# Kernel optimization log

Hardware: AMD Instinct MI355X
Metric: run time of the kernel (lower is better)

## Reference

```python
import jax, jax.numpy as jnp
import numpy as np

N = 100_000
E = 1_600_000
IN, HID, OUT, ED = 128, 128, 64, 16
NEG_SLOPE = 0.2  # PyG GATConv default leaky_relu slope


def segment_softmax(logits, seg, num_segments):
    m = jax.ops.segment_max(logits, seg, num_segments=num_segments)
    m = jnp.where(jnp.isfinite(m), m, 0.0)
    e = jnp.exp(logits - m[seg])
    s = jax.ops.segment_sum(e, seg, num_segments=num_segments)
    return e / (s[seg] + 1e-16)


def gat_conv(x, edge_index, W, a_src, a_dst, b, edge_attr=None, We=None, ae=None):
    """PyG GATConv, heads=1, add_self_loops=True, fill_value='mean'."""
    n = x.shape[0]
    h = x @ W  # [N, C]
    loop = jnp.arange(n, dtype=edge_index.dtype)
    src = jnp.concatenate([edge_index[0], loop])  # [E+N]
    dst = jnp.concatenate([edge_index[1], loop])
    alpha = (h * a_src).sum(-1)[src] + (h * a_dst).sum(-1)[dst]  # [E+N]
    if edge_attr is not None:
        # self-loop edge_attr filled with per-destination mean (PyG fill_value='mean')
        cnt = jax.ops.segment_sum(jnp.ones((edge_attr.shape[0],), edge_attr.dtype), edge_index[1], num_segments=n)
        mean_attr = jax.ops.segment_sum(edge_attr, edge_index[1], num_segments=n) / jnp.maximum(cnt, 1.0)[:, None]
        ea = jnp.concatenate([edge_attr, mean_attr], axis=0)  # [E+N, ED]
        alpha = alpha + (ea @ We) @ ae
    alpha = jax.nn.leaky_relu(alpha, NEG_SLOPE)
    alpha = segment_softmax(alpha, dst, n)
    out = jax.ops.segment_sum(alpha[:, None] * h[src], dst, num_segments=n)  # scatter-add
    return out + b


def setup_inputs() -> dict:
    key = jax.random.key(0)
    ks = iter(jax.random.split(key, 32))
    g = lambda shape, fan: (jax.random.normal(next(ks), shape, jnp.float32) * (1.0 / np.sqrt(fan)))
    inp = {
        "x": jax.random.normal(next(ks), (N, IN), jnp.float32),
        "edge_index": jax.random.randint(next(ks), (2, E), 0, N, jnp.int32),
        "edge_attr": jax.random.normal(next(ks), (E, ED), jnp.float32),
        # conv1 (no edge_attr)
        "W1": g((IN, HID), IN), "a1_src": g((HID,), HID), "a1_dst": g((HID,), HID), "b1": jnp.zeros((HID,), jnp.float32),
        # conv2 (with edge_attr)
        "W2": g((HID, HID), HID), "a2_src": g((HID,), HID), "a2_dst": g((HID,), HID), "b2": jnp.zeros((HID,), jnp.float32),
        "We2": g((ED, HID), ED), "ae2": g((HID,), HID),
        # initial residual linear
        "Wr": g((IN, HID), IN), "br": jnp.zeros((HID,), jnp.float32),
        # conv_mu
        "Wmu": g((HID, OUT), HID), "amu_src": g((OUT,), OUT), "amu_dst": g((OUT,), OUT), "bmu": jnp.zeros((OUT,), jnp.float32),
        "Wemu": g((ED, OUT), ED), "aemu": g((OUT,), OUT),
        # conv_logstd
        "Wls": g((HID, OUT), HID), "als_src": g((OUT,), OUT), "als_dst": g((OUT,), OUT), "bls": jnp.zeros((OUT,), jnp.float32),
        "Wels": g((ED, OUT), ED), "aels": g((OUT,), OUT),
    }
    return inp


def reference(x, edge_index, edge_attr,
              W1, a1_src, a1_dst, b1,
              W2, a2_src, a2_dst, b2, We2, ae2,
              Wr, br,
              Wmu, amu_src, amu_dst, bmu, Wemu, aemu,
              Wls, als_src, als_dst, bls, Wels, aels):
    h = jax.nn.relu(gat_conv(x, edge_index, W1, a1_src, a1_dst, b1))
    h = jax.nn.relu(gat_conv(h, edge_index, W2, a2_src, a2_dst, b2, edge_attr, We2, ae2))
    h = h + (x @ Wr + br)  # initial residual
    mu = gat_conv(h, edge_index, Wmu, amu_src, amu_dst, bmu, edge_attr, Wemu, aemu)
    logstd = gat_conv(h, edge_index, Wls, als_src, als_dst, bls, edge_attr, Wels, aels)
    return mu, logstd
```

## Files before the change

kernel.cpp:

```cpp
#include <hip/hip_runtime.h>

#define NN 100000
#define NE 1600000
#define BSH 9
#define NBUK 196

typedef __attribute__((ext_vector_type(8))) short bf16x8;
typedef __attribute__((ext_vector_type(4))) float f32x4;

__device__ __forceinline__ float wave_sum(float v){
  #pragma unroll
  for (int o = 32; o; o >>= 1) v += __shfl_xor(v, o, 64);
  return v;
}
__device__ __forceinline__ float grp_sum16(float v){
  #pragma unroll
  for (int o = 8; o; o >>= 1) v += __shfl_xor(v, o, 16);
  return v;
}
__device__ __forceinline__ float bf2f(unsigned short x){
  return __uint_as_float(((unsigned)x) << 16);
}
__device__ __forceinline__ unsigned short f2bf(float f){
  unsigned u = __float_as_uint(f);
  return (unsigned short)((u + 0x7FFFu + ((u >> 16) & 1u)) >> 16);
}

__global__ void prep_w_kernel(const float* __restrict__ W1, const float* __restrict__ W2,
                              const float* __restrict__ Wr, const float* __restrict__ Wmu,
                              const float* __restrict__ Wls,
                              unsigned short* __restrict__ W1t, unsigned short* __restrict__ W2t,
                              unsigned short* __restrict__ Wrt, unsigned short* __restrict__ Wmlt){
  int b = blockIdx.x, t = threadIdx.x;
  for (int it = 0; it < 64; it++){
    int idx = it*256 + t;
    int k = idx >> 7, c = idx & 127;
    float v; unsigned short* dst;
    if (b == 0){ v = W1[k*128+c]; dst = W1t; }
    else if (b == 1){ v = W2[k*128+c]; dst = W2t; }
    else if (b == 2){ v = Wr[k*128+c]; dst = Wrt; }
    else { v = (c & 1) ? Wls[k*64 + (c>>1)] : Wmu[k*64 + (c>>1)]; dst = Wmlt; }
    dst[c*128 + k] = f2bf(v);
  }
}

__global__ void wvec_kernel(const float* __restrict__ We2, const float* __restrict__ ae2,
                            const float* __restrict__ Wemu, const float* __restrict__ aemu,
                            const float* __restrict__ Wels, const float* __restrict__ aels,
                            float* __restrict__ wv){
  int t = threadIdx.x;
  if (t < 16){
    float s = 0.f; for (int c = 0; c < 128; c++) s += We2[t*128+c]*ae2[c];
    wv[t] = s;
  } else if (t < 32){
    int k = t-16; float s = 0.f; for (int c = 0; c < 64; c++) s += Wemu[k*64+c]*aemu[c];
    wv[16+k] = s;
  } else if (t < 48){
    int k = t-32; float s = 0.f; for (int c = 0; c < 64; c++) s += Wels[k*64+c]*aels[c];
    wv[32+k] = s;
  }
}

__global__ void cast_x_kernel(const float* __restrict__ x, unsigned short* __restrict__ Xb){
  int i = blockIdx.x*256 + threadIdx.x;
  if (i >= NN*128/8) return;
  const float4* src = (const float4*)x + (size_t)i*2;
  float4 v0 = src[0], v1 = src[1];
  ushort4 o0 = make_ushort4(f2bf(v0.x), f2bf(v0.y), f2bf(v0.z), f2bf(v0.w));
  ushort4 o1 = make_ushort4(f2bf(v1.x), f2bf(v1.y), f2bf(v1.z), f2bf(v1.w));
  *(ushort4*)(Xb + (size_t)i*8)     = o0;
  *(ushort4*)(Xb + (size_t)i*8 + 4) = o1;
}

__global__ void zero_kernel(int* __restrict__ p, int n){
  int i = blockIdx.x*256 + threadIdx.x;
  if (i < n) p[i] = 0;
}

__global__ __launch_bounds__(1024) void ehist_kernel(const int* __restrict__ ei,
                                                     unsigned* __restrict__ gbcnt){
  __shared__ unsigned h[256];
  int t = threadIdx.x;
  if (t < 256) h[t] = 0;
  __syncthreads();
  int e0 = blockIdx.x*4096 + t;
  #pragma unroll
  for (int k = 0; k < 4; k++){
    int e = e0 + k*1024;
    if (e < NE) atomicAdd(&h[ei[NE+e] >> BSH], 1);
  }
  __syncthreads();
  if (t < 256 && h[t]) atomicAdd(&gbcnt[t], h[t]);
}

__global__ void bscan_kernel(const unsigned* __restrict__ gbcnt,
                             unsigned* __restrict__ gbbase, int* __restrict__ rowptr){
  __shared__ unsigned sh[256];
  int t = threadIdx.x;
  unsigned v = gbcnt[t];
  sh[t] = v; __syncthreads();
  for (int o = 1; o < 256; o <<= 1){
    unsigned add = (t >= o) ? sh[t-o] : 0;
    __syncthreads();
    sh[t] += add;
    __syncthreads();
  }
  gbbase[t+1] = sh[t];
  if (t == 0){ gbbase[0] = 0; rowptr[NN] = NE; }
}

__global__ __launch_bounds__(1024) void bin_kernel(const int* __restrict__ ei,
                                                   const float* __restrict__ ea,
                                                   const float* __restrict__ wv,
                                                   const unsigned* __restrict__ gbbase,
                                                   unsigned* __restrict__ gbfill,
                                                   uint2* __restrict__ bdu,
                                                   float4* __restrict__ bw){
  __shared__ unsigned hcnt[256], hbase[256], hcur[256];
  __shared__ float wvs[48];
  int t = threadIdx.x;
  if (t < 256){ hcnt[t] = 0; hcur[t] = 0; }
  else if (t >= 256 && t < 304) wvs[t-256] = wv[t-256];
  __syncthreads();
  int d[4], u[4], b[4]; float4 w[4]; bool val[4];
  int e0 = blockIdx.x*4096 + t;
  #pragma unroll
  for (int k = 0; k < 4; k++){
    int e = e0 + k*1024;
    val[k] = e < NE;
    if (val[k]){
      d[k] = ei[NE+e]; u[k] = ei[e];
      b[k] = d[k] >> BSH;
      atomicAdd(&hcnt[b[k]], 1);
      const float4* p = (const float4*)(ea + (size_t)e*16);
      float a[16]; float4 vv;
      vv = p[0]; a[0]=vv.x; a[1]=vv.y; a[2]=vv.z; a[3]=vv.w;
      vv = p[1]; a[4]=vv.x; a[5]=vv.y; a[6]=vv.z; a[7]=vv.w;
      vv = p[2]; a[8]=vv.x; a[9]=vv.y; a[10]=vv.z; a[11]=vv.w;
      vv = p[3]; a[12]=vv.x; a[13]=vv.y; a[14]=vv.z; a[15]=vv.w;
      float s2 = 0.f, smu = 0.f, sls = 0.f;
      #pragma unroll
      for (int q = 0; q < 16; q++){
        s2  = fmaf(a[q], wvs[q],    s2);
        smu = fmaf(a[q], wvs[16+q], smu);
        sls = fmaf(a[q], wvs[32+q], sls);
      }
      w[k] = make_float4(s2, smu, sls, 0.f);
    }
  }
  __syncthreads();
  if (t < 256){
    unsigned c = hcnt[t];
    hbase[t] = c ? atomicAdd(&gbfill[t], c) : 0u;
  }
  __syncthreads();
  #pragma unroll
  for (int k = 0; k < 4; k++){
    if (val[k]){
      unsigned pos = atomicAdd(&hcur[b[k]], 1);
      unsigned slot = gbbase[b[k]] + hbase[b[k]] + pos;
      bdu[slot] = make_uint2((unsigned)d[k], (unsigned)u[k]);
      bw[slot]  = w[k];
    }
  }
}

__global__ __launch_bounds__(1024) void place_kernel(const uint2* __restrict__ bdu,
                                                     const float4* __restrict__ bw,
                                                     const unsigned* __restrict__ gbbase,
                                                     int* __restrict__ rowptr,
                                                     unsigned* __restrict__ csr_u,
                                                     float* __restrict__ ewp2,
                                                     float2* __restrict__ ewpmuls){
  __shared__ unsigned h[512], incl[512], cur[512];
  int b = blockIdx.x, t = threadIdx.x;
  unsigned cbase = gbbase[b];
  unsigned cnt = gbbase[b+1] - cbase;
  if (t < 512) h[t] = 0;
  __syncthreads();
  for (unsigned i = t; i < cnt; i += 1024)
    atomicAdd(&h[bdu[cbase+i].x & 511], 1);
  __syncthreads();
  if (t < 512) incl[t] = h[t];
  __syncthreads();
  for (int o = 1; o < 512; o <<= 1){
    unsigned add = (t >= o && t < 512) ? incl[t-o] : 0;
    __syncthreads();
    if (t < 512) incl[t] += add;
    __syncthreads();
  }
  if (t < 512){
    cur[t] = 0;
    int node = (b << BSH) + t;
    if (node < NN) rowptr[node] = (int)(cbase + incl[t] - h[t]);
  }
  __syncthreads();
  for (unsigned i = t; i < cnt; i += 1024){
    uint2 du = bdu[cbase+i];
    unsigned ld = du.x & 511;
    unsigned pos = atomicAdd(&cur[ld], 1);
    unsigned slot = cbase + (incl[ld] - h[ld]) + pos;
    float4 w = bw[cbase+i];
    csr_u[slot] = du.y;
    ewp2[slot] = w.x;
    ewpmuls[slot] = make_float2(w.y, w.z);
  }
}

template<bool OUTF32>
__global__ __launch_bounds__(256) void gemm_bf16(const unsigned short* __restrict__ Xb,
                                                 const unsigned short* __restrict__ Wt,
                                                 void* __restrict__ Y,
                                                 const float* __restrict__ bias, int nrows){
  __shared__ uint4 As[128*16];
  __shared__ uint4 Bs[128*16];
  int t = threadIdx.x;
  int row0 = blockIdx.x * 128;
  #pragma unroll
  for (int p = 0; p < 8; p++){
    int idx = p*256 + t;
    int r = idx >> 4, cir = idx & 15;
    uint4 v = make_uint4(0,0,0,0);
    if (row0 + r < nrows) v = *(const uint4*)(Xb + ((size_t)(row0+r))*128 + cir*8);
    As[r*16 + (cir ^ (r & 7))] = v;
  }
  #pragma unroll
  for (int p = 0; p < 8; p++){
    int idx = p*256 + t;
    int r = idx >> 4, cir = idx & 15;
    Bs[r*16 + (cir ^ (r & 7))] = *(const uint4*)(Wt + (size_t)r*128 + cir*8);
  }
  __syncthreads();
  int w = t >> 6, l = t & 63;
  int lr = l & 15;
  int lk = l >> 4;
  const bf16x8* As8 = (const bf16x8*)As;
  const bf16x8* Bs8 = (const bf16x8*)Bs;
  f32x4 acc[2][8];
  f32x4 zero = {0.f, 0.f, 0.f, 0.f};
  #pragma unroll
  for (int m = 0; m < 2; m++)
    #pragma unroll
    for (int n = 0; n < 8; n++) acc[m][n] = zero;
  #pragma unroll
  for (int ks = 0; ks < 4; ks++){
    bf16x8 a0, a1, bf[8];
    { int r = w*32 + lr;      a0 = As8[r*16 + ((ks*4+lk) ^ (r&7))]; }
    { int r = w*32 + 16 + lr; a1 = As8[r*16 + ((ks*4+lk) ^ (r&7))]; }
    #pragma unroll
    for (int nt = 0; nt < 8; nt++){
      int r = nt*16 + lr;
      bf[nt] = Bs8[r*16 + ((ks*4+lk) ^ (r&7))];
    }
    #pragma unroll
    for (int nt = 0; nt < 8; nt++){
      acc[0][nt] = __builtin_amdgcn_mfma_f32_16x16x32_bf16(a0, bf[nt], acc[0][nt], 0, 0, 0);
      acc[1][nt] = __builtin_amdgcn_mfma_f32_16x16x32_bf16(a1, bf[nt], acc[1][nt], 0, 0, 0);
    }
  }
  #pragma unroll
  for (int mt = 0; mt < 2; mt++){
    int gr0 = row0 + w*32 + mt*16 + lk*4;
    #pragma unroll
    for (int nt = 0; nt < 8; nt++){
      int col = nt*16 + lr;
      float bv = OUTF32 ? bias[col] : 0.f;
      #pragma unroll
      for (int i = 0; i < 4; i++){
        int r = gr0 + i;
        if (r < nrows){
          float o = acc[mt][nt][i];
          if constexpr (OUTF32) ((float*)Y)[(size_t)r*128 + col] = o + bv;
          else ((unsigned short*)Y)[(size_t)r*128 + col] = f2bf(o);
        }
      }
    }
  }
}

__global__ __launch_bounds__(256) void dots_kernel(const unsigned short* __restrict__ Hb,
                                                   const float* __restrict__ asrc,
                                                   const float* __restrict__ adst,
                                                   float* __restrict__ s, float* __restrict__ d){
  int n = (blockIdx.x * blockDim.x + threadIdx.x) >> 6;
  int lane = threadIdx.x & 63;
  if (n >= NN) return;
  ushort2 q = *(const ushort2*)(Hb + (size_t)n*128 + lane*2);
  float h0 = bf2f(q.x), h1 = bf2f(q.y);
  float ps = h0*asrc[lane*2] + h1*asrc[lane*2+1];
  float pd = h0*adst[lane*2] + h1*adst[lane*2+1];
  ps = wave_sum(ps); pd = wave_sum(pd);
  if (lane == 0){ s[n] = ps; d[n] = pd; }
}

__global__ __launch_bounds__(256) void dots_muls_kernel(const unsigned short* __restrict__ Yb,
                                                        const float* __restrict__ amus,
                                                        const float* __restrict__ amud,
                                                        const float* __restrict__ alss,
                                                        const float* __restrict__ alsd,
                                                        float2* __restrict__ sg,
                                                        float2* __restrict__ dg){
  int n = (blockIdx.x * blockDim.x + threadIdx.x) >> 6;
  int lane = threadIdx.x & 63;
  if (n >= NN) return;
  ushort2 q = *(const ushort2*)(Yb + (size_t)n*128 + lane*2);
  float hmu = bf2f(q.x), hls = bf2f(q.y);
  float smu = wave_sum(hmu * amus[lane]);
  float dmu = wave_sum(hmu * amud[lane]);
  float sls = wave_sum(hls * alss[lane]);
  float dls = wave_sum(hls * alsd[lane]);
  if (lane == 0){ sg[n] = make_float2(smu, sls); dg[n] = make_float2(dmu, dls); }
}

template<bool HAS_EW>
__global__ __launch_bounds__(256) void agg_conv(const unsigned short* __restrict__ Hb,
                                                const float* __restrict__ s,
                                                const float* __restrict__ dsc,
                                                const float* __restrict__ ewp,
                                                const int* __restrict__ rowptr,
                                                const unsigned* __restrict__ csr_u,
                                                const float* __restrict__ bias,
                                                const float* __restrict__ resid,
                                                unsigned short* __restrict__ out){
  int v = (blockIdx.x * blockDim.x + threadIdx.x) >> 4;
  int lig = threadIdx.x & 15;
  if (v >= NN) return;
  int rs = rowptr[v], re = rowptr[v+1];
  int deg = re - rs;
  float d_v = dsc[v];
  float acc[8] = {0.f,0.f,0.f,0.f,0.f,0.f,0.f,0.f};
  float pl = 0.f, ewl = 0.f;
  for (int base = rs; base < re; base += 16){
    int i = base + lig;
    int u = 0; float w = 0.f;
    if (i < re){
      u = (int)csr_u[i];
      float e = HAS_EW ? ewp[i] : 0.f;
      if (HAS_EW) ewl += e;
      float a = s[u] + d_v + e;
      float l = a > 0.f ? a : 0.2f*a;
      w = __expf(l);
    }
    pl += w;
    int nv = re - base; if (nv > 16) nv = 16;
    int j = 0;
    for (; j + 4 <= nv; j += 4){
      uint4 q[4]; float wj[4];
      #pragma unroll
      for (int k = 0; k < 4; k++){
        int uk = __shfl(u, j+k, 16);
        wj[k] = __shfl(w, j+k, 16);
        q[k] = *(const uint4*)(Hb + (size_t)uk*128 + lig*8);
      }
      #pragma unroll
      for (int k = 0; k < 4; k++){
        const unsigned* qq = (const unsigned*)&q[k];
        #pragma unroll
        for (int c = 0; c < 4; c++){
          acc[2*c]   = fmaf(wj[k], __uint_as_float(qq[c] << 16), acc[2*c]);
          acc[2*c+1] = fmaf(wj[k], __uint_as_float(qq[c] & 0xFFFF0000u), acc[2*c+1]);
        }
      }
    }
    for (; j < nv; j++){
      int uk = __shfl(u, j, 16);
      float wk = __shfl(w, j, 16);
      uint4 q = *(const uint4*)(Hb + (size_t)uk*128 + lig*8);
      const unsigned* qq = (const unsigned*)&q;
      #pragma unroll
      for (int c = 0; c < 4; c++){
        acc[2*c]   = fmaf(wk, __uint_as_float(qq[c] << 16), acc[2*c]);
        acc[2*c+1] = fmaf(wk, __uint_as_float(qq[c] & 0xFFFF0000u), acc[2*c+1]);
      }
    }
  }
  float p = grp_sum16(pl);
  float ews = HAS_EW ? grp_sum16(ewl) : 0.f;
  float selfa = s[v] + d_v + (HAS_EW ? ews / (float)(deg > 1 ? deg : 1) : 0.f);
  float lself = selfa > 0.f ? selfa : 0.2f*selfa;
  float wself = __expf(lself);
  p += wself;
  {
    uint4 q = *(const uint4*)(Hb + (size_t)v*128 + lig*8);
    const unsigned* qq = (const unsigned*)&q;
    #pragma unroll
    for (int c = 0; c < 4; c++){
      acc[2*c]   = fmaf(wself, __uint_as_float(qq[c] << 16), acc[2*c]);
      acc[2*c+1] = fmaf(wself, __uint_as_float(qq[c] & 0xFFFF0000u), acc[2*c+1]);
    }
  }
  float inv = 1.f / p;
  int c0 = lig*8;
  float o[8];
  #pragma unroll
  for (int c = 0; c < 8; c++){
    o[c] = acc[c]*inv + bias[c0+c];
    o[c] = fmaxf(o[c], 0.f);
  }
  if (HAS_EW){
    float4 r0 = *(const float4*)(resid + (size_t)v*128 + c0);
    float4 r1 = *(const float4*)(resid + (size_t)v*128 + c0 + 4);
    o[0]+=r0.x; o[1]+=r0.y; o[2]+=r0.z; o[3]+=r0.w;
    o[4]+=r1.x; o[5]+=r1.y; o[6]+=r1.z; o[7]+=r1.w;
  }
  uint4 ow;
  unsigned* owp = (unsigned*)&ow;
  #pragma unroll
  for (int c = 0; c < 4; c++)
    owp[c] = (unsigned)f2bf(o[2*c]) | ((unsigned)f2bf(o[2*c+1]) << 16);
  *(uint4*)(out + (size_t)v*128 + c0) = ow;
}

__global__ __launch_bounds__(256) void agg_muls(const unsigned short* __restrict__ Yb,
                                                const float2* __restrict__ sg,
                                                const float2* __restrict__ dg,
                                                const float2* __restrict__ ewpmuls,
                                                const int* __restrict__ rowptr,
                                                const unsigned* __restrict__ csr_u,
                                                const float* __restrict__ bmu,
                                                const float* __restrict__ bls,
                                                float* __restrict__ outmu,
                                                float* __restrict__ outls){
  int v = (blockIdx.x * blockDim.x + threadIdx.x) >> 4;
  int lig = threadIdx.x & 15;
  if (v >= NN) return;
  int rs = rowptr[v], re = rowptr[v+1];
  int deg = re - rs;
  float2 dv = dg[v];
  float accmu[4] = {0.f,0.f,0.f,0.f}, accls[4] = {0.f,0.f,0.f,0.f};
  float pmu = 0.f, pls = 0.f, ewlmu = 0.f, ewlls = 0.f;
  for (int base = rs; base < re; base += 16){
    int i = base + lig;
    int u = 0; float wmu = 0.f, wls = 0.f;
    if (i < re){
      u = (int)csr_u[i];
      float2 su = sg[u];
      float2 ee = ewpmuls[i];
      ewlmu += ee.x; ewlls += ee.y;
      float amu = su.x + dv.x + ee.x;
      float als = su.y + dv.y + ee.y;
      float lmu = amu > 0.f ? amu : 0.2f*amu;
      float lls = als > 0.f ? als : 0.2f*als;
      wmu = __expf(lmu); wls = __expf(lls);
    }
    pmu += wmu; pls += wls;
    int nv = re - base; if (nv > 16) nv = 16;
    int j = 0;
    for (; j + 4 <= nv; j += 4){
      uint4 q[4]; float wm[4], wl[4];
      #pragma unroll
      for (int k = 0; k < 4; k++){
        int uk = __shfl(u, j+k, 16);
        wm[k] = __shfl(wmu, j+k, 16);
        wl[k] = __shfl(wls, j+k, 16);
        q[k] = *(const uint4*)(Yb + (size_t)uk*128 + lig*8);
      }
      #pragma unroll
      for (int k = 0; k < 4; k++){
        const unsigned* qq = (const unsigned*)&q[k];
        #pragma unroll
        for (int c = 0; c < 4; c++){
          accmu[c] = fmaf(wm[k], __uint_as_float(qq[c] << 16), accmu[c]);
          accls[c] = fmaf(wl[k], __uint_as_float(qq[c] & 0xFFFF0000u), accls[c]);
        }
      }
    }
    for (; j < nv; j++){
      int uk = __shfl(u, j, 16);
      float wmk = __shfl(wmu, j, 16), wlk = __shfl(wls, j, 16);
      uint4 q = *(const uint4*)(Yb + (size_t)uk*128 + lig*8);
      const unsigned* qq = (const unsigned*)&q;
      #pragma unroll
      for (int c = 0; c < 4; c++){
        accmu[c] = fmaf(wmk, __uint_as_float(qq[c] << 16), accmu[c]);
        accls[c] = fmaf(wlk, __uint_as_float(qq[c] & 0xFFFF0000u), accls[c]);
      }
    }
  }
  float Pmu = grp_sum16(pmu), Pls = grp_sum16(pls);
  float Emu = grp_sum16(ewlmu), Els = grp_sum16(ewlls);
  float2 sv = sg[v];
  float dnm = (float)(deg > 1 ? deg : 1);
  float selfmu = sv.x + dv.x + Emu/dnm;
  float selfls = sv.y + dv.y + Els/dnm;
  float lmu = selfmu > 0.f ? selfmu : 0.2f*selfmu;
  float lls = selfls > 0.f ? selfls : 0.2f*selfls;
  float wmu_s = __expf(lmu), wls_s = __expf(lls);
  Pmu += wmu_s; Pls += wls_s;
  {
    uint4 q = *(const uint4*)(Yb + (size_t)v*128 + lig*8);
    const unsigned* qq = (const unsigned*)&q;
    #pragma unroll
    for (int c = 0; c < 4; c++){
      accmu[c] = fmaf(wmu_s, __uint_as_float(qq[c] << 16), accmu[c]);
      accls[c] = fmaf(wls_s, __uint_as_float(qq[c] & 0xFFFF0000u), accls[c]);
    }
  }
  float imu = 1.f/Pmu, ils = 1.f/Pls;
  int c0 = lig*4;
  float4 omu = make_float4(accmu[0]*imu + bmu[c0], accmu[1]*imu + bmu[c0+1],
                           accmu[2]*imu + bmu[c0+2], accmu[3]*imu + bmu[c0+3]);
  float4 ols = make_float4(accls[0]*ils + bls[c0], accls[1]*ils + bls[c0+1],
                           accls[2]*ils + bls[c0+2], accls[3]*ils + bls[c0+3]);
  *(float4*)(outmu + (size_t)v*64 + c0) = omu;
  *(float4*)(outls + (size_t)v*64 + c0) = ols;
}

extern "C" void kernel_launch(void* const* d_in, const int* in_sizes, int n_in,
                              void* d_out, int out_size, void* d_ws, size_t ws_size,
                              hipStream_t stream){
  const float* x    = (const float*)d_in[0];
  const int*   ei   = (const int*)  d_in[1];
  const float* ea   = (const float*)d_in[2];
  const float* W1   = (const float*)d_in[3];
  const float* a1s  = (const float*)d_in[4];
  const float* a1d  = (const float*)d_in[5];
  const float* b1   = (const float*)d_in[6];
  const float* W2   = (const float*)d_in[7];
  const float* a2s  = (const float*)d_in[8];
  const float* a2d  = (const float*)d_in[9];
  const float* b2   = (const float*)d_in[10];
  const float* We2  = (const float*)d_in[11];
  const float* ae2  = (const float*)d_in[12];
  const float* Wr   = (const float*)d_in[13];
  const float* br   = (const float*)d_in[14];
  const float* Wmu  = (const float*)d_in[15];
  const float* amus = (const float*)d_in[16];
  const float* amud = (const float*)d_in[17];
  const float* bmu  = (const float*)d_in[18];
  const float* Wemu = (const float*)d_in[19];
  const float* aemu = (const float*)d_in[20];
  const float* Wls  = (const float*)d_in[21];
  const float* alss = (const float*)d_in[22];
  const float* alsd = (const float*)d_in[23];
  const float* bls  = (const float*)d_in[24];
  const float* Wels = (const float*)d_in[25];
  const float* aels = (const float*)d_in[26];

  char* base = (char*)d_ws;
  size_t off = 0;
  auto alloc = [&](size_t bytes)->char*{
    char* p = base + off;
    off = (off + bytes + 511) & ~(size_t)511;
    return p;
  };
  int*      rowptr = (int*)   alloc((size_t)(NN+1)*4);
  unsigned* gbcnt  = (unsigned*)alloc(512*4);
  unsigned* gbfill = gbcnt + 256;
  unsigned* gbbase = (unsigned*)alloc(257*4);
  uint2*    bdu    = (uint2*) alloc((size_t)NE*8);
  float4*   bw     = (float4*)alloc((size_t)NE*16);
  unsigned* csr_u  = (unsigned*)alloc((size_t)NE*4);
  float*    ewp2   = (float*) alloc((size_t)NE*4);
  float2*   ewpmls = (float2*)alloc((size_t)NE*8);
  float*    wv     = (float*) alloc(48*4);
  float*    s1     = (float*) alloc((size_t)NN*4);
  float*    d1     = (float*) alloc((size_t)NN*4);
  float2*   sg2    = (float2*)alloc((size_t)NN*8);
  float2*   dg2    = (float2*)alloc((size_t)NN*8);
  unsigned short* W1t  = (unsigned short*)alloc(128*128*2);
  unsigned short* W2t  = (unsigned short*)alloc(128*128*2);
  unsigned short* Wrt  = (unsigned short*)alloc(128*128*2);
  unsigned short* Wmlt = (unsigned short*)alloc(128*128*2);
  unsigned short* Xb   = (unsigned short*)alloc((size_t)NN*128*2);
  unsigned short* bufA = (unsigned short*)alloc((size_t)NN*128*2);
  unsigned short* bufB = (unsigned short*)alloc((size_t)NN*128*2);
  if (off > ws_size) return;

  float* outF = (float*)d_out;
  float* muO  = outF;
  float* lsO  = outF + (size_t)NN*64;

  const int HB   = (NE + 4095)/4096;
  const int WB   = (NN*64 + 255)/256;
  const int WB16 = (NN*16 + 255)/256;
  const int GB   = (NN + 127)/128;
  const int CB   = (NN*128/8 + 255)/256;

  prep_w_kernel<<<4, 256, 0, stream>>>(W1, W2, Wr, Wmu, Wls, W1t, W2t, Wrt, Wmlt);
  wvec_kernel<<<1, 64, 0, stream>>>(We2, ae2, Wemu, aemu, Wels, aels, wv);
  cast_x_kernel<<<CB, 256, 0, stream>>>(x, Xb);
  zero_kernel<<<2, 256, 0, stream>>>((int*)gbcnt, 512);
  ehist_kernel<<<HB, 1024, 0, stream>>>(ei, gbcnt);
  bscan_kernel<<<1, 256, 0, stream>>>(gbcnt, gbbase, rowptr);
  bin_kernel<<<HB, 1024, 0, stream>>>(ei, ea, wv, gbbase, gbfill, bdu, bw);
  place_kernel<<<NBUK, 1024, 0, stream>>>(bdu, bw, gbbase, rowptr, csr_u, ewp2, ewpmls);

  gemm_bf16<false><<<GB, 256, 0, stream>>>(Xb, W1t, bufA, nullptr, NN);
  dots_kernel<<<WB, 256, 0, stream>>>(bufA, a1s, a1d, s1, d1);
  agg_conv<false><<<WB16, 256, 0, stream>>>(bufA, s1, d1, nullptr, rowptr, csr_u,
                                            b1, nullptr, bufB);
  gemm_bf16<false><<<GB, 256, 0, stream>>>(bufB, W2t, bufA, nullptr, NN);
  dots_kernel<<<WB, 256, 0, stream>>>(bufA, a2s, a2d, s1, d1);
  gemm_bf16<true><<<GB, 256, 0, stream>>>(Xb, Wrt, outF, br, NN);
  agg_conv<true><<<WB16, 256, 0, stream>>>(bufA, s1, d1, ewp2, rowptr, csr_u,
                                           b2, outF, bufB);
  gemm_bf16<false><<<GB, 256, 0, stream>>>(bufB, Wmlt, bufA, nullptr, NN);
  dots_muls_kernel<<<WB, 256, 0, stream>>>(bufA, amus, amud, alss, alsd, sg2, dg2);
  agg_muls<<<WB16, 256, 0, stream>>>(bufA, sg2, dg2, ewpmls, rowptr, csr_u,
                                     bmu, bls, muO, lsO);
}
```

Before: 490.6 us.

## Fuse attention dot products into GEMM epilogue and widen aggregation to 32 lanes

Computes the per-node source/destination attention scores inside the bf16 MFMA GEMM epilogue using the fp32 accumulators, removing the separate dots kernels and their re-read of the hidden features. The aggregation kernels now assign 32 lanes per node with 8-byte gathers and process neighbors in batches of 8 without a tail loop. Padded slots rely on zero weights and dummy loads of row 0. This trades the extra kernel passes for more lanes per node and some wasted gather loads on low-degree nodes.

```diff
diff --git a/kernel.cpp b/kernel.cpp
--- a/kernel.cpp
+++ b/kernel.cpp
@@ -8,14 +8,14 @@
 typedef __attribute__((ext_vector_type(8))) short bf16x8;
 typedef __attribute__((ext_vector_type(4))) float f32x4;
 
-__device__ __forceinline__ float wave_sum(float v){
-  #pragma unroll
-  for (int o = 32; o; o >>= 1) v += __shfl_xor(v, o, 64);
+__device__ __forceinline__ float grp_sum16(float v){
+  #pragma unroll
+  for (int o = 8; o; o >>= 1) v += __shfl_xor(v, o, 16);
   return v;
 }
-__device__ __forceinline__ float grp_sum16(float v){
-  #pragma unroll
-  for (int o = 8; o; o >>= 1) v += __shfl_xor(v, o, 16);
+__device__ __forceinline__ float grp_sum32(float v){
+  #pragma unroll
+  for (int o = 16; o; o >>= 1) v += __shfl_xor(v, o, 32);
   return v;
 }
 __device__ __forceinline__ float bf2f(unsigned short x){
@@ -207,11 +207,17 @@
   }
 }
 
-template<bool OUTF32>
+template<bool OUTF32, int DOTS>
 __global__ __launch_bounds__(256) void gemm_bf16(const unsigned short* __restrict__ Xb,
                                                  const unsigned short* __restrict__ Wt,
                                                  void* __restrict__ Y,
-                                                 const float* __restrict__ bias, int nrows){
+                                                 const float* __restrict__ bias, int nrows,
+                                                 const float* __restrict__ va,
+                                                 const float* __restrict__ vb,
+                                                 const float* __restrict__ vc,
+                                                 const float* __restrict__ vd,
+                                                 float* __restrict__ sOut,
+                                                 float* __restrict__ dOut){
   __shared__ uint4 As[128*16];
   __shared__ uint4 Bs[128*16];
   int t = threadIdx.x;
@@ -258,6 +264,49 @@
       acc[1][nt] = __builtin_amdgcn_mfma_f32_16x16x32_bf16(a1, bf[nt], acc[1][nt], 0, 0, 0);
     }
   }
+  if constexpr (DOTS == 1){
+    #pragma unroll
+    for (int mt = 0; mt < 2; mt++){
+      #pragma unroll
+      for (int i = 0; i < 4; i++){
+        float ps = 0.f, pd = 0.f;
+        #pragma unroll
+        for (int nt = 0; nt < 8; nt++){
+          float av = acc[mt][nt][i];
+          int col = nt*16 + lr;
+          ps = fmaf(av, va[col], ps);
+          pd = fmaf(av, vb[col], pd);
+        }
+        ps = grp_sum16(ps); pd = grp_sum16(pd);
+        int r = row0 + w*32 + mt*16 + lk*4 + i;
+        if (lr == 0 && r < nrows){ sOut[r] = ps; dOut[r] = pd; }
+      }
+    }
+  }
+  if constexpr (DOTS == 2){
+    #pragma unroll
+    for (int mt = 0; mt < 2; mt++){
+      #pragma unroll
+      for (int i = 0; i < 4; i++){
+        float pmu = 0.f, pdm = 0.f, pls = 0.f, pdl = 0.f;
+        #pragma unroll
+        for (int nt = 0; nt < 8; nt++){
+          float av = acc[mt][nt][i];
+          int col = nt*16 + lr;
+          int c = col >> 1;
+          if (col & 1){ pls = fmaf(av, vc[c], pls); pdl = fmaf(av, vd[c], pdl); }
+          else        { pmu = fmaf(av, va[c], pmu); pdm = fmaf(av, vb[c], pdm); }
+        }
+        pmu = grp_sum16(pmu); pdm = grp_sum16(pdm);
+        pls = grp_sum16(pls); pdl = grp_sum16(pdl);
+        int r = row0 + w*32 + mt*16 + lk*4 + i;
+        if (lr == 0 && r < nrows){
+          ((float2*)sOut)[r] = make_float2(pmu, pls);
+          ((float2*)dOut)[r] = make_float2(pdm, pdl);
+        }
+      }
+    }
+  }
   #pragma unroll
   for (int mt = 0; mt < 2; mt++){
     int gr0 = row0 + w*32 + mt*16 + lk*4;
@@ -276,40 +325,6 @@
       }
     }
   }
-}
-
-__global__ __launch_bounds__(256) void dots_kernel(const unsigned short* __restrict__ Hb,
-                                                   const float* __restrict__ asrc,
-                                                   const float* __restrict__ adst,
-                                                   float* __restrict__ s, float* __restrict__ d){
-  int n = (blockIdx.x * blockDim.x + threadIdx.x) >> 6;
-  int lane = threadIdx.x & 63;
-  if (n >= NN) return;
-  ushort2 q = *(const ushort2*)(Hb + (size_t)n*128 + lane*2);
-  float h0 = bf2f(q.x), h1 = bf2f(q.y);
-  float ps = h0*asrc[lane*2] + h1*asrc[lane*2+1];
-  float pd = h0*adst[lane*2] + h1*adst[lane*2+1];
-  ps = wave_sum(ps); pd = wave_sum(pd);
-  if (lane == 0){ s[n] = ps; d[n] = pd; }
-}
-
-__global__ __launch_bounds__(256) void dots_muls_kernel(const unsigned short* __restrict__ Yb,
-                                                        const float* __restrict__ amus,
-                                                        const float* __restrict__ amud,
-                                                        const float* __restrict__ alss,
-                                                        const float* __restrict__ alsd,
-                                                        float2* __restrict__ sg,
-                                                        float2* __restrict__ dg){
-  int n = (blockIdx.x * blockDim.x + threadIdx.x) >> 6;
-  int lane = threadIdx.x & 63;
-  if (n >= NN) return;
-  ushort2 q = *(const ushort2*)(Yb + (size_t)n*128 + lane*2);
-  float hmu = bf2f(q.x), hls = bf2f(q.y);
-  float smu = wave_sum(hmu * amus[lane]);
-  float dmu = wave_sum(hmu * amud[lane]);
-  float sls = wave_sum(hls * alss[lane]);
-  float dls = wave_sum(hls * alsd[lane]);
-  if (lane == 0){ sg[n] = make_float2(smu, sls); dg[n] = make_float2(dmu, dls); }
 }
 
 template<bool HAS_EW>
@@ -322,15 +337,15 @@
                                                 const float* __restrict__ bias,
                                                 const float* __restrict__ resid,
                                                 unsigned short* __restrict__ out){
-  int v = (blockIdx.x * blockDim.x + threadIdx.x) >> 4;
-  int lig = threadIdx.x & 15;
+  int v = (blockIdx.x * blockDim.x + threadIdx.x) >> 5;
+  int lig = threadIdx.x & 31;
   if (v >= NN) return;
   int rs = rowptr[v], re = rowptr[v+1];
   int deg = re - rs;
   float d_v = dsc[v];
-  float acc[8] = {0.f,0.f,0.f,0.f,0.f,0.f,0.f,0.f};
+  float acc[4] = {0.f,0.f,0.f,0.f};
   float pl = 0.f, ewl = 0.f;
-  for (int base = rs; base < re; base += 16){
+  for (int base = rs; base < re; base += 32){
     int i = base + lig;
     int u = 0; float w = 0.f;
     if (i < re){
@@ -342,73 +357,52 @@
       w = __expf(l);
     }
     pl += w;
-    int nv = re - base; if (nv > 16) nv = 16;
-    int j = 0;
-    for (; j + 4 <= nv; j += 4){
-      uint4 q[4]; float wj[4];
-      #pragma unroll
-      for (int k = 0; k < 4; k++){
-        int uk = __shfl(u, j+k, 16);
-        wj[k] = __shfl(w, j+k, 16);
-        q[k] = *(const uint4*)(Hb + (size_t)uk*128 + lig*8);
-      }
-      #pragma unroll
-      for (int k = 0; k < 4; k++){
-        const unsigned* qq = (const unsigned*)&q[k];
-        #pragma unroll
-        for (int c = 0; c < 4; c++){
-          acc[2*c]   = fmaf(wj[k], __uint_as_float(qq[c] << 16), acc[2*c]);
-          acc[2*c+1] = fmaf(wj[k], __uint_as_float(qq[c] & 0xFFFF0000u), acc[2*c+1]);
-        }
-      }
-    }
-    for (; j < nv; j++){
-      int uk = __shfl(u, j, 16);
-      float wk = __shfl(w, j, 16);
-      uint4 q = *(const uint4*)(Hb + (size_t)uk*128 + lig*8);
-      const unsigned* qq = (const unsigned*)&q;
-      #pragma unroll
-      for (int c = 0; c < 4; c++){
-        acc[2*c]   = fmaf(wk, __uint_as_float(qq[c] << 16), acc[2*c]);
-        acc[2*c+1] = fmaf(wk, __uint_as_float(qq[c] & 0xFFFF0000u), acc[2*c+1]);
-      }
-    }
-  }
-  float p = grp_sum16(pl);
-  float ews = HAS_EW ? grp_sum16(ewl) : 0.f;
+    int nv = re - base; if (nv > 32) nv = 32;
+    for (int j = 0; j < nv; j += 8){
+      uint2 q[8]; float wj[8];
+      #pragma unroll
+      for (int k = 0; k < 8; k++){
+        int uk = __shfl(u, j+k, 32);
+        wj[k] = __shfl(w, j+k, 32);
+        q[k] = *(const uint2*)(Hb + (size_t)uk*128 + lig*4);
+      }
+      #pragma unroll
+      for (int k = 0; k < 8; k++){
+        acc[0] = fmaf(wj[k], __uint_as_float(q[k].x << 16), acc[0]);
+        acc[1] = fmaf(wj[k], __uint_as_float(q[k].x & 0xFFFF0000u), acc[1]);
+        acc[2] = fmaf(wj[k], __uint_as_float(q[k].y << 16), acc[2]);
+        acc[3] = fmaf(wj[k], __uint_as_float(q[k].y & 0xFFFF0000u), acc[3]);
+      }
+    }
+  }
+  float p = grp_sum32(pl);
+  float ews = HAS_EW ? grp_sum32(ewl) : 0.f;
   float selfa = s[v] + d_v + (HAS_EW ? ews / (float)(deg > 1 ? deg : 1) : 0.f);
   float lself = selfa > 0.f ? selfa : 0.2f*selfa;
   float wself = __expf(lself);
   p += wself;
   {
-    uint4 q = *(const uint4*)(Hb + (size_t)v*128 + lig*8);
-    const unsigned* qq = (const unsigned*)&q;
-    #pragma unroll
-    for (int c = 0; c < 4; c++){
-      acc[2*c]   = fmaf(wself, __uint_as_float(qq[c] << 16), acc[2*c]);
-      acc[2*c+1] = fmaf(wself, __uint_as_float(qq[c] & 0xFFFF0000u), acc[2*c+1]);
-    }
+    uint2 q = *(const uint2*)(Hb + (size_t)v*128 + lig*4);
+    acc[0] = fmaf(wself, __uint_as_float(q.x << 16), acc[0]);
+    acc[1] = fmaf(wself, __uint_as_float(q.x & 0xFFFF0000u), acc[1]);
+    acc[2] = fmaf(wself, __uint_as_float(q.y << 16), acc[2]);
+    acc[3] = fmaf(wself, __uint_as_float(q.y & 0xFFFF0000u), acc[3]);
   }
   float inv = 1.f / p;
-  int c0 = lig*8;
-  float o[8];
-  #pragma unroll
-  for (int c = 0; c < 8; c++){
-    o[c] = acc[c]*inv + bias[c0+c];
-    o[c] = fmaxf(o[c], 0.f);
-  }
+  int c0 = lig*4;
+  float4 bv = *(const float4*)(bias + c0);
+  float o0 = fmaxf(acc[0]*inv + bv.x, 0.f);
+  float o1 = fmaxf(acc[1]*inv + bv.y, 0.f);
+  float o2 = fmaxf(acc[2]*inv + bv.z, 0.f);
+  float o3 = fmaxf(acc[3]*inv + bv.w, 0.f);
   if (HAS_EW){
     float4 r0 = *(const float4*)(resid + (size_t)v*128 + c0);
-    float4 r1 = *(const float4*)(resid + (size_t)v*128 + c0 + 4);
-    o[0]+=r0.x; o[1]+=r0.y; o[2]+=r0.z; o[3]+=r0.w;
-    o[4]+=r1.x; o[5]+=r1.y; o[6]+=r1.z; o[7]+=r1.w;
-  }
-  uint4 ow;
-  unsigned* owp = (unsigned*)&ow;
-  #pragma unroll
-  for (int c = 0; c < 4; c++)
-    owp[c] = (unsigned)f2bf(o[2*c]) | ((unsigned)f2bf(o[2*c+1]) << 16);
-  *(uint4*)(out + (size_t)v*128 + c0) = ow;
+    o0 += r0.x; o1 += r0.y; o2 += r0.z; o3 += r0.w;
+  }
+  uint2 ow;
+  ow.x = (unsigned)f2bf(o0) | ((unsigned)f2bf(o1) << 16);
+  ow.y = (unsigned)f2bf(o2) | ((unsigned)f2bf(o3) << 16);
+  *(uint2*)(out + (size_t)v*128 + c0) = ow;
 }
 
 __global__ __launch_bounds__(256) void agg_muls(const unsigned short* __restrict__ Yb,
@@ -421,15 +415,15 @@
                                                 const float* __restrict__ bls,
                                                 float* __restrict__ outmu,
                                                 float* __restrict__ outls){
-  int v = (blockIdx.x * blockDim.x + threadIdx.x) >> 4;
-  int lig = threadIdx.x & 15;
+  int v = (blockIdx.x * blockDim.x + threadIdx.x) >> 5;
+  int lig = threadIdx.x & 31;
   if (v >= NN) return;
   int rs = rowptr[v], re = rowptr[v+1];
   int deg = re - rs;
   float2 dv = dg[v];
-  float accmu[4] = {0.f,0.f,0.f,0.f}, accls[4] = {0.f,0.f,0.f,0.f};
+  float accmu[2] = {0.f,0.f}, accls[2] = {0.f,0.f};
   float pmu = 0.f, pls = 0.f, ewlmu = 0.f, ewlls = 0.f;
-  for (int base = rs; base < re; base += 16){
+  for (int base = rs; base < re; base += 32){
     int i = base + lig;
     int u = 0; float wmu = 0.f, wls = 0.f;
     if (i < re){
@@ -444,41 +438,27 @@
       wmu = __expf(lmu); wls = __expf(lls);
     }
     pmu += wmu; pls += wls;
-    int nv = re - base; if (nv > 16) nv = 16;
-    int j = 0;
-    for (; j + 4 <= nv; j += 4){
-      uint4 q[4]; float wm[4], wl[4];
-      #pragma unroll
-      for (int k = 0; k < 4; k++){
-        int uk = __shfl(u, j+k, 16);
-        wm[k] = __shfl(wmu, j+k, 16);
-        wl[k] = __shfl(wls, j+k, 16);
-        q[k] = *(const uint4*)(Yb + (size_t)uk*128 + lig*8);
-      }
-      #pragma unroll
-      for (int k = 0; k < 4; k++){
-        const unsigned* qq = (const unsigned*)&q[k];
-        #pragma unroll
-        for (int c = 0; c < 4; c++){
-          accmu[c] = fmaf(wm[k], __uint_as_float(qq[c] << 16), accmu[c]);
-          accls[c] = fmaf(wl[k], __uint_as_float(qq[c] & 0xFFFF0000u), accls[c]);
-        }
-      }
-    }
-    for (; j < nv; j++){
-      int uk = __shfl(u, j, 16);
-      float wmk = __shfl(wmu, j, 16), wlk = __shfl(wls, j, 16);
-      uint4 q = *(const uint4*)(Yb + (size_t)uk*128 + lig*8);
-      const unsigned* qq = (const unsigned*)&q;
-      #pragma unroll
-      for (int c = 0; c < 4; c++){
-        accmu[c] = fmaf(wmk, __uint_as_float(qq[c] << 16), accmu[c]);
-        accls[c] = fmaf(wlk, __uint_as_float(qq[c] & 0xFFFF0000u), accls[c]);
-      }
-    }
-  }
-  float Pmu = grp_sum16(pmu), Pls = grp_sum16(pls);
-  float Emu = grp_sum16(ewlmu), Els = grp_sum16(ewlls);
+    int nv = re - base; if (nv > 32) nv = 32;
+    for (int j = 0; j < nv; j += 8){
+      uint2 q[8]; float wm[8], wl[8];
+      #pragma unroll
+      for (int k = 0; k < 8; k++){
+        int uk = __shfl(u, j+k, 32);
+        wm[k] = __shfl(wmu, j+k, 32);
+        wl[k] = __shfl(wls, j+k, 32);
+        q[k] = *(const uint2*)(Yb + (size_t)uk*128 + lig*4);
+      }
+      #pragma unroll
+      for (int k = 0; k < 8; k++){
+        accmu[0] = fmaf(wm[k], __uint_as_float(q[k].x << 16), accmu[0]);
+        accls[0] = fmaf(wl[k], __uint_as_float(q[k].x & 0xFFFF0000u), accls[0]);
+        accmu[1] = fmaf(wm[k], __uint_as_float(q[k].y << 16), accmu[1]);
+        accls[1] = fmaf(wl[k], __uint_as_float(q[k].y & 0xFFFF0000u), accls[1]);
+      }
+    }
+  }
+  float Pmu = grp_sum32(pmu), Pls = grp_sum32(pls);
+  float Emu = grp_sum32(ewlmu), Els = grp_sum32(ewlls);
   float2 sv = sg[v];
   float dnm = (float)(deg > 1 ? deg : 1);
   float selfmu = sv.x + dv.x + Emu/dnm;
@@ -488,22 +468,18 @@
   float wmu_s = __expf(lmu), wls_s = __expf(lls);
   Pmu += wmu_s; Pls += wls_s;
   {
-    uint4 q = *(const uint4*)(Yb + (size_t)v*128 + lig*8);
-    const unsigned* qq = (const unsigned*)&q;
-    #pragma unroll
-    for (int c = 0; c < 4; c++){
-      accmu[c] = fmaf(wmu_s, __uint_as_float(qq[c] << 16), accmu[c]);
-      accls[c] = fmaf(wls_s, __uint_as_float(qq[c] & 0xFFFF0000u), accls[c]);
-    }
+    uint2 q = *(const uint2*)(Yb + (size_t)v*128 + lig*4);
+    accmu[0] = fmaf(wmu_s, __uint_as_float(q.x << 16), accmu[0]);
+    accls[0] = fmaf(wls_s, __uint_as_float(q.x & 0xFFFF0000u), accls[0]);
+    accmu[1] = fmaf(wmu_s, __uint_as_float(q.y << 16), accmu[1]);
+    accls[1] = fmaf(wls_s, __uint_as_float(q.y & 0xFFFF0000u), accls[1]);
   }
   float imu = 1.f/Pmu, ils = 1.f/Pls;
-  int c0 = lig*4;
-  float4 omu = make_float4(accmu[0]*imu + bmu[c0], accmu[1]*imu + bmu[c0+1],
-                           accmu[2]*imu + bmu[c0+2], accmu[3]*imu + bmu[c0+3]);
-  float4 ols = make_float4(accls[0]*ils + bls[c0], accls[1]*ils + bls[c0+1],
-                           accls[2]*ils + bls[c0+2], accls[3]*ils + bls[c0+3]);
-  *(float4*)(outmu + (size_t)v*64 + c0) = omu;
-  *(float4*)(outls + (size_t)v*64 + c0) = ols;
+  int c0 = lig*2;
+  float2 omu = make_float2(accmu[0]*imu + bmu[c0], accmu[1]*imu + bmu[c0+1]);
+  float2 ols = make_float2(accls[0]*ils + bls[c0], accls[1]*ils + bls[c0+1]);
+  *(float2*)(outmu + (size_t)v*64 + c0) = omu;
+  *(float2*)(outls + (size_t)v*64 + c0) = ols;
 }
 
 extern "C" void kernel_launch(void* const* d_in, const int* in_sizes, int n_in,
@@ -572,8 +548,7 @@
   float* lsO  = outF + (size_t)NN*64;
 
   const int HB   = (NE + 4095)/4096;
-  const int WB   = (NN*64 + 255)/256;
-  const int WB16 = (NN*16 + 255)/256;
+  const int WB32 = (NN*32 + 255)/256;
   const int GB   = (NN + 127)/128;
   const int CB   = (NN*128/8 + 255)/256;
 
@@ -586,17 +561,20 @@
   bin_kernel<<<HB, 1024, 0, stream>>>(ei, ea, wv, gbbase, gbfill, bdu, bw);
   place_kernel<<<NBUK, 1024, 0, stream>>>(bdu, bw, gbbase, rowptr, csr_u, ewp2, ewpmls);
 
-  gemm_bf16<false><<<GB, 256, 0, stream>>>(Xb, W1t, bufA, nullptr, NN);
-  dots_kernel<<<WB, 256, 0, stream>>>(bufA, a1s, a1d, s1, d1);
-  agg_conv<false><<<WB16, 256, 0, stream>>>(bufA, s1, d1, nullptr, rowptr, csr_u,
+  gemm_bf16<false,1><<<GB, 256, 0, stream>>>(Xb, W1t, bufA, nullptr, NN,
+                                             a1s, a1d, nullptr, nullptr, s1, d1);
+  agg_conv<false><<<WB32, 256, 0, stream>>>(bufA, s1, d1, nullptr, rowptr, csr_u,
                                             b1, nullptr, bufB);
-  gemm_bf16<false><<<GB, 256, 0, stream>>>(bufB, W2t, bufA, nullptr, NN);
-  dots_kernel<<<WB, 256, 0, stream>>>(bufA, a2s, a2d, s1, d1);
-  gemm_bf16<true><<<GB, 256, 0, stream>>>(Xb, Wrt, outF, br, NN);
-  agg_conv<true><<<WB16, 256, 0, stream>>>(bufA, s1, d1, ewp2, rowptr, csr_u,
+  gemm_bf16<false,1><<<GB, 256, 0, stream>>>(bufB, W2t, bufA, nullptr, NN,
+                                             a2s, a2d, nullptr, nullptr, s1, d1);
+  gemm_bf16<true,0><<<GB, 256, 0, stream>>>(Xb, Wrt, outF, br, NN,
+                                            nullptr, nullptr, nullptr, nullptr,
+                                            nullptr, nullptr);
+  agg_conv<true><<<WB32, 256, 0, stream>>>(bufA, s1, d1, ewp2, rowptr, csr_u,
                                            b2, outF, bufB);
-  gemm_bf16<false><<<GB, 256, 0, stream>>>(bufB, Wmlt, bufA, nullptr, NN);
-  dots_muls_kernel<<<WB, 256, 0, stream>>>(bufA, amus, amud, alss, alsd, sg2, dg2);
-  agg_muls<<<WB16, 256, 0, stream>>>(bufA, sg2, dg2, ewpmls, rowptr, csr_u,
+  gemm_bf16<false,2><<<GB, 256, 0, stream>>>(bufB, Wmlt, bufA, nullptr, NN,
+                                             amus, amud, alss, alsd,
+                                             (float*)sg2, (float*)dg2);
+  agg_muls<<<WB32, 256, 0, stream>>>(bufA, sg2, dg2, ewpmls, rowptr, csr_u,
                                      bmu, bls, muO, lsO);
 }
```

Measured after the change: 453.1 us. 7.6% less time.
